# Performance work log

Hardware: AMD Instinct MI355X
Metric: run time of the kernel (lower is better)

The kernel has to match this reference:

```python
import jax, jax.numpy as jnp
import numpy as np

S = 1024   # qlen = klen (mems=None)
B = 4
D = 1024   # d_model
N = 16     # n_head
H = 64     # d_head
R = 2 * S  # relative position embedding length = klen + qlen
EPS = 1e-12
SCALE = float(1.0 / np.sqrt(H))


def setup_inputs() -> dict:
    key = jax.random.key(0)
    ks = jax.random.split(key, 14)
    h = jax.random.normal(ks[0], (S, B, D), dtype=jnp.float32)
    r = jax.random.normal(ks[1], (R, B, D), dtype=jnp.float32)
    # segment ids -> one-hot same/diff segment matrix [i, j, b, 2]
    seg_ids = jax.random.randint(ks[2], (S, B), 0, 2)
    diff = (seg_ids[:, None, :] != seg_ids[None, :, :]).astype(jnp.int32)  # [S,S,B]
    seg_mat = jax.nn.one_hot(diff, 2, dtype=jnp.float32)  # [S,S,B,2]
    # causal attention mask: 1 where key position j > query position i
    causal = (jnp.arange(S)[None, :] > jnp.arange(S)[:, None]).astype(jnp.float32)
    attn_mask = jnp.broadcast_to(causal[:, :, None, None], (S, S, B, 1))
    w = lambda k, shape: 0.02 * jax.random.normal(k, shape, dtype=jnp.float32)
    return {
        "h": h, "r": r, "seg_mat": seg_mat, "attn_mask": attn_mask,
        "Wq": w(ks[3], (D, N, H)), "Wk": w(ks[4], (D, N, H)),
        "Wv": w(ks[5], (D, N, H)), "Wo": w(ks[6], (D, N, H)),
        "Wr": w(ks[7], (D, N, H)),
        "r_w_bias": w(ks[8], (N, H)), "r_r_bias": w(ks[9], (N, H)),
        "r_s_bias": w(ks[10], (N, H)), "seg_embed": w(ks[11], (2, N, H)),
        "ln_scale": jnp.ones((D,), jnp.float32), "ln_bias": jnp.zeros((D,), jnp.float32),
    }


def rel_shift_bnij(x, klen):
    # x: [b, n, i, j_r] with j_r = klen + qlen
    b, n, i, j = x.shape
    x = x.reshape(b, n, j, i)[:, :, 1:, :].reshape(b, n, i, j - 1)
    return x[:, :, :, :klen]


def layer_norm(x, scale, bias):
    mu = jnp.mean(x, axis=-1, keepdims=True)
    var = jnp.mean(jnp.square(x - mu), axis=-1, keepdims=True)
    return (x - mu) * jax.lax.rsqrt(var + EPS) * scale + bias


def reference(h, r, seg_mat, attn_mask, Wq, Wk, Wv, Wo, Wr,
              r_w_bias, r_r_bias, r_s_bias, seg_embed, ln_scale, ln_bias):
    # projections (mems=None => cat = h)
    q_head = jnp.einsum('ibh,hnd->ibnd', h, Wq)
    k_head_h = jnp.einsum('ibh,hnd->ibnd', h, Wk)
    v_head_h = jnp.einsum('ibh,hnd->ibnd', h, Wv)
    k_head_r = jnp.einsum('ibh,hnd->ibnd', r, Wr)

    klen = k_head_h.shape[0]
    # content-based score
    ac = jnp.einsum('ibnd,jbnd->bnij', q_head + r_w_bias, k_head_h)
    # position-based score with relative shift
    bd = jnp.einsum('ibnd,jbnd->bnij', q_head + r_r_bias, k_head_r)
    bd = rel_shift_bnij(bd, klen)
    # segment-based score
    ef = jnp.einsum('ibnd,snd->ibns', q_head + r_s_bias, seg_embed)
    ef = jnp.einsum('ijbs,ibns->bnij', seg_mat, ef)

    attn_score = (ac + bd + ef) * SCALE
    attn_score = attn_score - 1e30 * jnp.transpose(attn_mask, (2, 3, 0, 1))  # ijbn->bnij
    attn_prob = jax.nn.softmax(attn_score, axis=3)

    attn_vec = jnp.einsum('bnij,jbnd->ibnd', attn_prob, v_head_h)
    attn_out = jnp.einsum('ibnd,hnd->ibh', attn_vec, Wo) + h  # residual
    return layer_norm(attn_out, ln_scale, ln_bias)
```

## Files before the change

kernel.cpp:

```cpp
#include <hip/hip_runtime.h>

#define Sq 1024
#define Bb 4
#define Dm 1024
#define Nh 16
#define Hd 64

typedef unsigned short ushort_t;
typedef __attribute__((ext_vector_type(8))) short s8v;
typedef __attribute__((ext_vector_type(8))) unsigned short us8;
typedef __attribute__((ext_vector_type(4))) float f32x4;
typedef __attribute__((ext_vector_type(2))) __fp16 fp16x2;

__device__ __forceinline__ float bf2f(ushort_t u) {
  union { unsigned int i; float f; } t; t.i = ((unsigned int)u) << 16; return t.f;
}
__device__ __forceinline__ ushort_t f2bf(float f) {
  union { float f; unsigned int i; } t; t.f = f;
  unsigned int lsb = (t.i >> 16) & 1u;
  t.i += 0x7fffu + lsb;
  return (ushort_t)(t.i >> 16);
}

__device__ __forceinline__ void load4(const float* p, float* o) {
  const float4 v = *(const float4*)p;
  o[0] = v.x; o[1] = v.y; o[2] = v.z; o[3] = v.w;
}

__device__ __forceinline__ float wave_reduce_sum(float v) {
#pragma unroll
  for (int off = 32; off; off >>= 1) v += __shfl_xor(v, off, 64);
  return v;
}

__device__ __forceinline__ void gl_lds16(const ushort_t* g, ushort_t* l) {
  __builtin_amdgcn_global_load_lds(
      (const __attribute__((address_space(1))) unsigned int*)g,
      (__attribute__((address_space(3))) unsigned int*)l, 16, 0, 0);
}

template <int MODE>
__device__ __forceinline__ void gemm128(const ushort_t* __restrict__ A,
                                        const ushort_t* __restrict__ B,
                                        void* __restrict__ Cv,
                                        const float* __restrict__ bias0,
                                        int bm, int bn,
                                        ushort_t* __restrict__ As,
                                        ushort_t* __restrict__ Bs) {
  const int tid = threadIdx.x;
  const int w = tid >> 6, lane = tid & 63;
  const int quad = lane >> 4, l16 = lane & 15;
  const int wm = (w & 1) * 64, wn = (w >> 1) * 64;
  const int srow0 = 32 * w + (lane >> 2);
  const int scb = (lane & 3) * 16;
  f32x4 acc[4][4] = {};

  for (int k0 = 0; k0 < 1024; k0 += 32) {
    __syncthreads();
#pragma unroll
    for (int c = 0; c < 2; ++c) {
      const int row = srow0 + c * 16;
      const int cbs = scb ^ (((row >> 1) & 3) << 4);
      gl_lds16(A + (size_t)(bm + row) * 1024 + k0 + (cbs >> 1),
               &As[(32 * w + c * 16) * 32]);
      gl_lds16(B + (size_t)(bn + row) * 1024 + k0 + (cbs >> 1),
               &Bs[(32 * w + c * 16) * 32]);
    }
    __syncthreads();
    s8v av[4], bv[4];
    const int sw = ((l16 >> 1) & 3) << 4;
    const int cbb = ((quad * 16) ^ sw) >> 1;
#pragma unroll
    for (int i = 0; i < 4; ++i) {
      av[i] = *(const s8v*)&As[(wm + i * 16 + l16) * 32 + cbb];
      bv[i] = *(const s8v*)&Bs[(wn + i * 16 + l16) * 32 + cbb];
    }
#pragma unroll
    for (int i = 0; i < 4; ++i)
#pragma unroll
      for (int j = 0; j < 4; ++j)
        acc[i][j] = __builtin_amdgcn_mfma_f32_16x16x32_bf16(av[i], bv[j], acc[i][j], 0, 0, 0);
  }

  float bj[4];
  if (MODE == 3) {
#pragma unroll
    for (int j = 0; j < 4; ++j) bj[j] = bias0[bn + wn + j * 16 + l16];
  }
#pragma unroll
  for (int i = 0; i < 4; ++i) {
#pragma unroll
    for (int j = 0; j < 4; ++j) {
      const int cg = bn + wn + j * 16 + l16;
#pragma unroll
      for (int reg = 0; reg < 4; ++reg) {
        const int mg = bm + wm + i * 16 + quad * 4 + reg;
        const float v = acc[i][j][reg];
        if (MODE == 3) {
          ((ushort_t*)Cv)[((size_t)(cg >> 6) * 1024 + mg) * 64 + (cg & 63)] =
              f2bf((v + bj[j]) * 0.125f);
        } else if (MODE == 0) {
          ((ushort_t*)Cv)[((size_t)(cg >> 6) * 1024 + mg) * 64 + (cg & 63)] = f2bf(v);
        } else if (MODE == 2) {
          const int m = cg & 63;
          const int cp = (cg & ~63) | ((m & 15) * 4 + (m >> 4));
          ((ushort_t*)Cv)[(size_t)mg * 1024 + cp] = f2bf(v);
        } else {
          ((float*)Cv)[(size_t)mg * 1024 + cg] = v + bias0[(size_t)mg * 1024 + cg];
        }
      }
    }
  }
}

__global__ __launch_bounds__(256) void prep(
    const float* __restrict__ h, const float* __restrict__ r,
    const float* __restrict__ Wq, const float* __restrict__ Wk,
    const float* __restrict__ Wv, const float* __restrict__ Wr,
    const float* __restrict__ Wo, const float* __restrict__ seg_mat,
    const float* __restrict__ rwb, const float* __restrict__ rrb,
    ushort_t* __restrict__ h_bf, ushort_t* __restrict__ r_bf,
    ushort_t* __restrict__ Wt, ushort_t* __restrict__ Wo_bf,
    float* __restrict__ sseg, float* __restrict__ drr) {
  __shared__ float t[64][68];
  const int x = blockIdx.x, y = blockIdx.y, tid = threadIdx.x;
  if (y < 4) {
    const int b = y, i = x, d0 = tid * 4;
    {
      const float4 v = *(const float4*)&h[(size_t)(i * 4 + b) * 1024 + d0];
      ushort4 o; o.x = f2bf(v.x); o.y = f2bf(v.y); o.z = f2bf(v.z); o.w = f2bf(v.w);
      *(ushort4*)&h_bf[(size_t)b * 1048576 + (size_t)i * 1024 + d0] = o;
    }
    {
      const float4 v = *(const float4*)&r[(size_t)(i * 4 + 4 + b) * 1024 + d0];
      ushort4 o; o.x = f2bf(v.x); o.y = f2bf(v.y); o.z = f2bf(v.z); o.w = f2bf(v.w);
      *(ushort4*)&r_bf[(size_t)b * 1048576 + (size_t)i * 1024 + d0] = o;
    }
    if (b == 0) {
      const float4 v = *(const float4*)&Wo[(size_t)i * 1024 + d0];
      ushort4 o; o.x = f2bf(v.x); o.y = f2bf(v.y); o.z = f2bf(v.z); o.w = f2bf(v.w);
      *(ushort4*)&Wo_bf[(size_t)i * 1024 + d0] = o;
      if (x < 16) {
        const int idx = x * 256 + tid;
        const int bb = idx >> 10, j = idx & 1023;
        sseg[bb * 1024 + j] = seg_mat[(size_t)j * 8 + bb * 2 + 1];
        if (idx < 1024) drr[idx] = (rrb[idx] - rwb[idx]) * 0.125f;
      }
    }
  } else {
    const int z = x >> 8, sub = x & 255;
    const float* W = (z == 0) ? Wq : (z == 1) ? Wk : (z == 2) ? Wv : Wr;
    ushort_t* O = Wt + (size_t)z * 1048576;
    const int n0 = (sub & 15) * 64, k0 = (sub >> 4) * 64;
    const int tr = tid >> 4, tc = (tid & 15) * 4;
#pragma unroll
    for (int rr = 0; rr < 4; ++rr) {
      const int r_ = tr + rr * 16;
      const float4 v = *(const float4*)&W[(size_t)(k0 + r_) * 1024 + n0 + tc];
      t[r_][tc] = v.x; t[r_][tc + 1] = v.y; t[r_][tc + 2] = v.z; t[r_][tc + 3] = v.w;
    }
    __syncthreads();
#pragma unroll
    for (int rr = 0; rr < 4; ++rr) {
      const int nr = tr + rr * 16;
      ushort4 o;
      o.x = f2bf(t[tc + 0][nr]); o.y = f2bf(t[tc + 1][nr]);
      o.z = f2bf(t[tc + 2][nr]); o.w = f2bf(t[tc + 3][nr]);
      *(ushort4*)&O[(size_t)(n0 + nr) * 1024 + k0 + tc] = o;
    }
  }
}

__global__ __launch_bounds__(256) void projAV(
    const ushort_t* __restrict__ h_bf, const ushort_t* __restrict__ r_bf,
    const ushort_t* __restrict__ Wt, const float* __restrict__ rwb,
    ushort_t* __restrict__ qcS, ushort_t* __restrict__ KSl,
    ushort_t* __restrict__ KRS, ushort_t* __restrict__ VTP) {
  __shared__ ushort_t As[128 * 32];
  __shared__ ushort_t Bs[128 * 32];
  const int z = blockIdx.z, zz = z & 3, b = z >> 2;
  const size_t slab = (size_t)Nh * Sq * Hd;
  const int bm = blockIdx.y * 128, bn = blockIdx.x * 128;
  if (zz == 0) {
    gemm128<3>(h_bf + (size_t)b * 1048576, Wt, qcS + b * slab, rwb, bm, bn, As, Bs);
  } else if (zz == 1) {
    gemm128<0>(h_bf + (size_t)b * 1048576, Wt + 1048576, KSl + b * slab,
               nullptr, bm, bn, As, Bs);
  } else if (zz == 2) {
    gemm128<2>(Wt + (size_t)2 * 1048576, h_bf + (size_t)b * 1048576,
               VTP + b * slab, nullptr, bm, bn, As, Bs);
  } else {
    gemm128<0>(r_bf + (size_t)b * 1048576, Wt + (size_t)3 * 1048576,
               KRS + b * slab, nullptr, bm, bn, As, Bs);
  }
}

__global__ __launch_bounds__(128) void attn_mfma(
    const ushort_t* __restrict__ QCS, const ushort_t* __restrict__ KS,
    const ushort_t* __restrict__ VTS, const ushort_t* __restrict__ KRS,
    const float* __restrict__ rwb, const float* __restrict__ rsb,
    const float* __restrict__ seg_embed, const float* __restrict__ sseg,
    const float* __restrict__ drr, ushort_t* __restrict__ AVbf) {
  const int nb = blockIdx.x;
  const int n = nb & 15, b = nb >> 4;
  const int i0b = (int)(gridDim.y - 1 - blockIdx.y) * 32;
  const int tid = threadIdx.x;
  const int w = tid >> 6;
  const int lane = tid & 63;
  const int quad = lane >> 4, l16 = lane & 15;
  const size_t slab = (size_t)Nh * Sq * Hd;
  const size_t nS = (size_t)n * Sq;
  const ushort_t* Qh = QCS + b * slab + nS * Hd;
  const ushort_t* Kh = KS + b * slab + nS * Hd;
  const ushort_t* Vh = VTS + b * slab + (size_t)n * Hd * Sq;
  const ushort_t* KRh = KRS + b * slab + nS * Hd;
  const float* ssegb = sseg + b * Sq;

  __shared__ ushort_t P_s[2][32 * 64];
  __shared__ float o_s[2][32][66];
  __shared__ float l_s[2][32];

  s8v qc[2][2], qr[2][2];
  float efa_v[2], efb_v[2];
  {
    float p0[2] = {0.f, 0.f}, p1[2] = {0.f, 0.f};
#pragma unroll
    for (int ks = 0; ks < 2; ++ks) {
      const int dl = ks * 32 + quad * 8;
      const int db = n * 64 + dl;
      float dr8[8], w8[8], s8a[8], e08[8], e18[8];
      load4(drr + db, dr8); load4(drr + db + 4, dr8 + 4);
      load4(rwb + db, w8);  load4(rwb + db + 4, w8 + 4);
      load4(rsb + db, s8a); load4(rsb + db + 4, s8a + 4);
      load4(seg_embed + db, e08); load4(seg_embed + db + 4, e08 + 4);
      load4(seg_embed + Nh * 64 + db, e18); load4(seg_embed + Nh * 64 + db + 4, e18 + 4);
#pragma unroll
      for (int sub = 0; sub < 2; ++sub) {
        const s8v qv = *(const s8v*)&Qh[(size_t)(i0b + sub * 16 + l16) * 64 + dl];
        qc[sub][ks] = qv;
#pragma unroll
        for (int e = 0; e < 8; ++e) {
          const float qcf = bf2f((ushort_t)qv[e]);
          qr[sub][ks][e] = (short)f2bf(qcf + dr8[e]);
          const float qs = qcf * 8.f - w8[e] + s8a[e];
          p0[sub] += qs * e08[e];
          p1[sub] += qs * e18[e];
        }
      }
    }
#pragma unroll
    for (int sub = 0; sub < 2; ++sub) {
      p0[sub] += __shfl_xor(p0[sub], 16, 64); p0[sub] += __shfl_xor(p0[sub], 32, 64);
      p1[sub] += __shfl_xor(p1[sub], 16, 64); p1[sub] += __shfl_xor(p1[sub], 32, 64);
      const float si = ssegb[i0b + sub * 16 + l16];
      const float de = p1[sub] - p0[sub];
      efa_v[sub] = (p0[sub] + de * si) * 0.125f;
      efb_v[sub] = de * (1.f - 2.f * si) * 0.125f;
    }
  }

  float efa_r[2][4], efb_r[2][4];
  int bp_idx[4], selhi[4];
#pragma unroll
  for (int reg = 0; reg < 4; ++reg) {
    const int il = quad * 4 + reg;
#pragma unroll
    for (int sub = 0; sub < 2; ++sub) {
      efa_r[sub][reg] = __shfl(efa_v[sub], il, 64);
      efb_r[sub][reg] = __shfl(efb_v[sub], il, 64);
    }
    const int off = l16 + 15 - il;
    bp_idx[reg] = (((quad << 4) | (off & 15)) << 2);
    selhi[reg] = off >> 4;
  }

  f32x4 o[2][4] = {};
  float l_r[2][4] = {};
  char* Pb = (char*)P_s[w];

  const int n_jt = i0b / 64 + 1;
  for (int jt = w; jt < n_jt; jt += 2) {
    const int j0 = jt * 64;
    const bool last = (jt == n_jt - 1);

    f32x4 sc[2][4];
    const ushort_t* Kt = Kh + (size_t)j0 * 64;
#pragma unroll
    for (int u = 0; u < 4; ++u) {
      const int ro = (u * 16 + l16) * 64 + quad * 8;
      const s8v k0v = *(const s8v*)&Kt[ro];
      const s8v k1v = *(const s8v*)&Kt[ro + 32];
#pragma unroll
      for (int sub = 0; sub < 2; ++sub) {
        f32x4 a = {};
        a = __builtin_amdgcn_mfma_f32_16x16x32_bf16(qc[sub][0], k0v, a, 0, 0, 0);
        a = __builtin_amdgcn_mfma_f32_16x16x32_bf16(qc[sub][1], k1v, a, 0, 0, 0);
        sc[sub][u] = a;
      }
    }

    f32x4 bdw[2][5];
    const int base1 = 992 + j0 - i0b;
#pragma unroll
    for (int f = 0; f < 6; ++f) {
      int g = base1 + f * 16 + l16;
      if (g > 1023) g = 1023;
      const int ro = g * 64 + quad * 8;
      const s8v r0v = *(const s8v*)&KRh[ro];
      const s8v r1v = *(const s8v*)&KRh[ro + 32];
      if (f < 5) {
        f32x4 a = {};
        a = __builtin_amdgcn_mfma_f32_16x16x32_bf16(qr[1][0], r0v, a, 0, 0, 0);
        a = __builtin_amdgcn_mfma_f32_16x16x32_bf16(qr[1][1], r1v, a, 0, 0, 0);
        bdw[1][f] = a;
      }
      if (f >= 1) {
        f32x4 a = {};
        a = __builtin_amdgcn_mfma_f32_16x16x32_bf16(qr[0][0], r0v, a, 0, 0, 0);
        a = __builtin_amdgcn_mfma_f32_16x16x32_bf16(qr[0][1], r1v, a, 0, 0, 0);
        bdw[0][f - 1] = a;
      }
    }

    float sj[4];
#pragma unroll
    for (int u = 0; u < 4; ++u) sj[u] = ssegb[j0 + u * 16 + l16];
#pragma unroll
    for (int sub = 0; sub < 2; ++sub) {
      float p[4][4];
#pragma unroll
      for (int u = 0; u < 4; ++u) {
#pragma unroll
        for (int reg = 0; reg < 4; ++reg) {
          const fp16x2 t = __builtin_amdgcn_cvt_pkrtz(bdw[sub][u][reg], bdw[sub][u + 1][reg]);
          const int g = __builtin_amdgcn_ds_bpermute(bp_idx[reg], __builtin_bit_cast(int, t));
          const __fp16 hf =
              __builtin_bit_cast(__fp16, (unsigned short)(selhi[reg] ? (g >> 16) : g));
          p[u][reg] = __expf(sc[sub][u][reg] + (float)hf + efa_r[sub][reg] +
                             efb_r[sub][reg] * sj[u]);
        }
      }
      if (last) {
#pragma unroll
        for (int u = 0; u < 4; ++u)
#pragma unroll
          for (int reg = 0; reg < 4; ++reg)
            if (j0 + u * 16 + l16 > i0b + sub * 16 + quad * 4 + reg) p[u][reg] = 0.f;
      }
#pragma unroll
      for (int reg = 0; reg < 4; ++reg)
        l_r[sub][reg] += p[0][reg] + p[1][reg] + p[2][reg] + p[3][reg];

#pragma unroll
      for (int reg = 0; reg < 4; ++reg) {
        const int i = sub * 16 + quad * 4 + reg;
        const unsigned int lo =
            (unsigned int)f2bf(p[0][reg]) | ((unsigned int)f2bf(p[1][reg]) << 16);
        const unsigned int hi =
            (unsigned int)f2bf(p[2][reg]) | ((unsigned int)f2bf(p[3][reg]) << 16);
        *(uint2*)(Pb + i * 128 + ((((l16 >> 1) ^ (i & 7)) << 4) | ((l16 & 1) << 3))) =
            make_uint2(lo, hi);
      }
    }

    s8v pa[2][2];
#pragma unroll
    for (int sub = 0; sub < 2; ++sub)
#pragma unroll
      for (int ks = 0; ks < 2; ++ks)
        pa[sub][ks] = *(const s8v*)(Pb + (sub * 16 + l16) * 128 +
                                    (((ks * 4 + quad) ^ (l16 & 7)) << 4));

    const ushort_t* Vt = Vh + j0;
#pragma unroll
    for (int u = 0; u < 4; ++u) {
      const size_t vro = (size_t)(u * 16 + l16) * Sq + quad * 8;
      const s8v v0 = *(const s8v*)&Vt[vro];
      const s8v v1 = *(const s8v*)&Vt[vro + 32];
#pragma unroll
      for (int sub = 0; sub < 2; ++sub) {
        o[sub][u] = __builtin_amdgcn_mfma_f32_16x16x32_bf16(pa[sub][0], v0, o[sub][u], 0, 0, 0);
        o[sub][u] = __builtin_amdgcn_mfma_f32_16x16x32_bf16(pa[sub][1], v1, o[sub][u], 0, 0, 0);
      }
    }
  }

#pragma unroll
  for (int sub = 0; sub < 2; ++sub)
#pragma unroll
    for (int reg = 0; reg < 4; ++reg) {
#pragma unroll
      for (int off = 1; off < 16; off <<= 1)
        l_r[sub][reg] += __shfl_xor(l_r[sub][reg], off, 64);
    }
  if (l16 == 0) {
#pragma unroll
    for (int sub = 0; sub < 2; ++sub)
#pragma unroll
      for (int reg = 0; reg < 4; ++reg)
        l_s[w][sub * 16 + quad * 4 + reg] = l_r[sub][reg];
  }
#pragma unroll
  for (int sub = 0; sub < 2; ++sub)
#pragma unroll
    for (int u = 0; u < 4; ++u)
#pragma unroll
      for (int reg = 0; reg < 4; ++reg)
        o_s[w][sub * 16 + quad * 4 + reg][u * 16 + l16] = o[sub][u][reg];
  __syncthreads();

  {
    const int row = tid >> 2;
    const int c0 = (tid & 3) * 16;
    const float lt = l_s[0][row] + l_s[1][row];
    const float inv = 1.0f / lt;
    const size_t base = ((size_t)(i0b + row) * Bb + b) * 1024 + n * 64;
#pragma unroll
    for (int half = 0; half < 2; ++half) {
      us8 ob;
#pragma unroll
      for (int e = 0; e < 8; ++e) {
        const int c = c0 + half * 8 + e;
        ob[e] = f2bf((o_s[0][row][c] + o_s[1][row][c]) * inv);
      }
      *(us8*)&AVbf[base + c0 + half * 8] = ob;
    }
  }
}

__global__ __launch_bounds__(256) void ln_res(float* __restrict__ out,
                                              const float* __restrict__ scale,
                                              const float* __restrict__ bias) {
  const int row = blockIdx.x;
  const int tid = threadIdx.x;
  __shared__ float red1[4], red2[4];
  float v[4];
  float sum = 0.f;
#pragma unroll
  for (int c = 0; c < 4; ++c) {
    const int idx = tid + c * 256;
    const float x = out[(size_t)row * Dm + idx];
    v[c] = x;
    sum += x;
  }
  sum = wave_reduce_sum(sum);
  const int wid = tid >> 6, lane = tid & 63;
  if (!lane) red1[wid] = sum;
  __syncthreads();
  const float mean = (red1[0] + red1[1] + red1[2] + red1[3]) * (1.0f / 1024.0f);
  float sq = 0.f;
#pragma unroll
  for (int c = 0; c < 4; ++c) {
    const float t = v[c] - mean;
    sq += t * t;
  }
  sq = wave_reduce_sum(sq);
  if (!lane) red2[wid] = sq;
  __syncthreads();
  const float var = (red2[0] + red2[1] + red2[2] + red2[3]) * (1.0f / 1024.0f);
  const float rstd = rsqrtf(var + 1e-12f);
#pragma unroll
  for (int c = 0; c < 4; ++c) {
    const int idx = tid + c * 256;
    out[(size_t)row * Dm + idx] = (v[c] - mean) * rstd * scale[idx] + bias[idx];
  }
}

__global__ __launch_bounds__(256) void outproj128(const ushort_t* __restrict__ AV,
                                                  const ushort_t* __restrict__ Wo,
                                                  const float* __restrict__ h,
                                                  float* __restrict__ AO) {
  __shared__ ushort_t As[128 * 32];
  __shared__ ushort_t Bs[128 * 32];
  gemm128<1>(AV, Wo, AO, h, blockIdx.y * 128, blockIdx.x * 128, As, Bs);
}

extern "C" void kernel_launch(void* const* d_in, const int* in_sizes, int n_in,
                              void* d_out, int out_size, void* d_ws, size_t ws_size,
                              hipStream_t stream) {
  const float* h = (const float*)d_in[0];
  const float* r = (const float*)d_in[1];
  const float* seg_mat = (const float*)d_in[2];
  const float* Wq = (const float*)d_in[4];
  const float* Wk = (const float*)d_in[5];
  const float* Wv = (const float*)d_in[6];
  const float* Wo = (const float*)d_in[7];
  const float* Wr = (const float*)d_in[8];
  const float* rwb = (const float*)d_in[9];
  const float* rrb = (const float*)d_in[10];
  const float* rsb = (const float*)d_in[11];
  const float* seg_embed = (const float*)d_in[12];
  const float* ln_scale = (const float*)d_in[13];
  const float* ln_bias = (const float*)d_in[14];

  char* wsb = (char*)d_ws;
  const size_t MB = 1024 * 1024;
  ushort_t* h_bf = (ushort_t*)(wsb + 0);
  ushort_t* r_bf = (ushort_t*)(wsb + 8 * MB);
  ushort_t* Wt = (ushort_t*)(wsb + 16 * MB);
  ushort_t* Wo_bf = (ushort_t*)(wsb + 24 * MB);
  ushort_t* qcS = (ushort_t*)(wsb + 26 * MB);
  ushort_t* KSl = (ushort_t*)(wsb + 34 * MB);
  ushort_t* VTP = (ushort_t*)(wsb + 42 * MB);
  ushort_t* KRS = (ushort_t*)(wsb + 50 * MB);
  float* sseg = (float*)(wsb + 58 * MB);
  float* drr = (float*)(wsb + 58 * MB + 16 * 1024);
  ushort_t* AVbf = h_bf;
  float* out = (float*)d_out;

  prep<<<dim3(1024, 5), 256, 0, stream>>>(h, r, Wq, Wk, Wv, Wr, Wo, seg_mat,
                                          rwb, rrb, h_bf, r_bf, Wt, Wo_bf, sseg, drr);
  projAV<<<dim3(8, 8, 16), 256, 0, stream>>>(h_bf, r_bf, Wt, rwb, qcS, KSl, KRS, VTP);
  attn_mfma<<<dim3(64, 32), 128, 0, stream>>>(qcS, KSl, VTP, KRS, rwb, rsb,
                                              seg_embed, sseg, drr, AVbf);
  outproj128<<<dim3(8, 32), 256, 0, stream>>>(AVbf, Wo_bf, h, out);
  ln_res<<<4096, 256, 0, stream>>>(out, ln_scale, ln_bias);
}
```

Baseline: 316.5 us.

## Process key tiles in pairs per wave to overlap softmax with loads

```diff
diff --git a/kernel.cpp b/kernel.cpp
--- a/kernel.cpp
+++ b/kernel.cpp
@@ -195,6 +195,53 @@
   }
 }
 
+__device__ __forceinline__ void softmax_tile(
+    const f32x4 (&sc)[2][4], const f32x4 (&bdw)[2][5],
+    const float* __restrict__ ssegb, int jbase, bool last_t, int i0b,
+    const float (&efa_r)[2][4], const float (&efb_r)[2][4],
+    const int (&bp_idx)[4], const int (&selhi)[4],
+    int quad, int l16, float (&l_r)[2][4], char* Pb) {
+  float sj[4];
+#pragma unroll
+  for (int u = 0; u < 4; ++u) sj[u] = ssegb[jbase + u * 16 + l16];
+#pragma unroll
+  for (int sub = 0; sub < 2; ++sub) {
+    float p[4][4];
+#pragma unroll
+    for (int u = 0; u < 4; ++u) {
+#pragma unroll
+      for (int reg = 0; reg < 4; ++reg) {
+        const fp16x2 t = __builtin_amdgcn_cvt_pkrtz(bdw[sub][u][reg], bdw[sub][u + 1][reg]);
+        const int g = __builtin_amdgcn_ds_bpermute(bp_idx[reg], __builtin_bit_cast(int, t));
+        const __fp16 hf =
+            __builtin_bit_cast(__fp16, (unsigned short)(selhi[reg] ? (g >> 16) : g));
+        p[u][reg] = __expf(sc[sub][u][reg] + (float)hf + efa_r[sub][reg] +
+                           efb_r[sub][reg] * sj[u]);
+      }
+    }
+    if (last_t) {
+#pragma unroll
+      for (int u = 0; u < 4; ++u)
+#pragma unroll
+        for (int reg = 0; reg < 4; ++reg)
+          if (jbase + u * 16 + l16 > i0b + sub * 16 + quad * 4 + reg) p[u][reg] = 0.f;
+    }
+#pragma unroll
+    for (int reg = 0; reg < 4; ++reg)
+      l_r[sub][reg] += p[0][reg] + p[1][reg] + p[2][reg] + p[3][reg];
+#pragma unroll
+    for (int reg = 0; reg < 4; ++reg) {
+      const int i = sub * 16 + quad * 4 + reg;
+      const unsigned int lo =
+          (unsigned int)f2bf(p[0][reg]) | ((unsigned int)f2bf(p[1][reg]) << 16);
+      const unsigned int hi =
+          (unsigned int)f2bf(p[2][reg]) | ((unsigned int)f2bf(p[3][reg]) << 16);
+      *(uint2*)(Pb + i * 128 + ((((l16 >> 1) ^ (i & 7)) << 4) | ((l16 & 1) << 3))) =
+          make_uint2(lo, hi);
+    }
+  }
+}
+
 __global__ __launch_bounds__(128) void attn_mfma(
     const ushort_t* __restrict__ QCS, const ushort_t* __restrict__ KS,
     const ushort_t* __restrict__ VTS, const ushort_t* __restrict__ KRS,
@@ -216,7 +263,7 @@
   const ushort_t* KRh = KRS + b * slab + nS * Hd;
   const float* ssegb = sseg + b * Sq;
 
-  __shared__ ushort_t P_s[2][32 * 64];
+  __shared__ ushort_t P_s[2][2][32 * 64];
   __shared__ float o_s[2][32][66];
   __shared__ float l_s[2][32];
 
@@ -276,111 +323,126 @@
 
   f32x4 o[2][4] = {};
   float l_r[2][4] = {};
-  char* Pb = (char*)P_s[w];
 
   const int n_jt = i0b / 64 + 1;
-  for (int jt = w; jt < n_jt; jt += 2) {
-    const int j0 = jt * 64;
-    const bool last = (jt == n_jt - 1);
-
-    f32x4 sc[2][4];
-    const ushort_t* Kt = Kh + (size_t)j0 * 64;
-#pragma unroll
-    for (int u = 0; u < 4; ++u) {
-      const int ro = (u * 16 + l16) * 64 + quad * 8;
-      const s8v k0v = *(const s8v*)&Kt[ro];
-      const s8v k1v = *(const s8v*)&Kt[ro + 32];
-#pragma unroll
-      for (int sub = 0; sub < 2; ++sub) {
-        f32x4 a = {};
-        a = __builtin_amdgcn_mfma_f32_16x16x32_bf16(qc[sub][0], k0v, a, 0, 0, 0);
-        a = __builtin_amdgcn_mfma_f32_16x16x32_bf16(qc[sub][1], k1v, a, 0, 0, 0);
-        sc[sub][u] = a;
-      }
-    }
-
-    f32x4 bdw[2][5];
-    const int base1 = 992 + j0 - i0b;
-#pragma unroll
-    for (int f = 0; f < 6; ++f) {
-      int g = base1 + f * 16 + l16;
-      if (g > 1023) g = 1023;
-      const int ro = g * 64 + quad * 8;
-      const s8v r0v = *(const s8v*)&KRh[ro];
-      const s8v r1v = *(const s8v*)&KRh[ro + 32];
-      if (f < 5) {
-        f32x4 a = {};
-        a = __builtin_amdgcn_mfma_f32_16x16x32_bf16(qr[1][0], r0v, a, 0, 0, 0);
-        a = __builtin_amdgcn_mfma_f32_16x16x32_bf16(qr[1][1], r1v, a, 0, 0, 0);
-        bdw[1][f] = a;
-      }
-      if (f >= 1) {
-        f32x4 a = {};
-        a = __builtin_amdgcn_mfma_f32_16x16x32_bf16(qr[0][0], r0v, a, 0, 0, 0);
-        a = __builtin_amdgcn_mfma_f32_16x16x32_bf16(qr[0][1], r1v, a, 0, 0, 0);
-        bdw[0][f - 1] = a;
-      }
-    }
-
-    float sj[4];
-#pragma unroll
-    for (int u = 0; u < 4; ++u) sj[u] = ssegb[j0 + u * 16 + l16];
-#pragma unroll
-    for (int sub = 0; sub < 2; ++sub) {
-      float p[4][4];
+  for (int jp = w; 2 * jp < n_jt; jp += 2) {
+    const int j0 = jp * 128;
+    const bool have2 = (2 * jp + 1) < n_jt;
+
+    f32x4 sc[2][2][4];
+#pragma unroll
+    for (int t2 = 0; t2 < 2; ++t2) {
+      if (t2 == 0 || have2) {
+        const ushort_t* Kt = Kh + (size_t)(j0 + t2 * 64) * 64;
+#pragma unroll
+        for (int u = 0; u < 4; ++u) {
+          const int ro = (u * 16 + l16) * 64 + quad * 8;
+          const s8v k0v = *(const s8v*)&Kt[ro];
+          const s8v k1v = *(const s8v*)&Kt[ro + 32];
+#pragma unroll
+          for (int sub = 0; sub < 2; ++sub) {
+            f32x4 a = {};
+            a = __builtin_amdgcn_mfma_f32_16x16x32_bf16(qc[sub][0], k0v, a, 0, 0, 0);
+            a = __builtin_amdgcn_mfma_f32_16x16x32_bf16(qc[sub][1], k1v, a, 0, 0, 0);
+            sc[t2][sub][u] = a;
+          }
+        }
+      }
+    }
+
+    f32x4 bdw[2][2][5];
+    const int base_pair = 992 + j0 - i0b;
+#pragma unroll
+    for (int f = 0; f < 10; ++f) {
+      if (f < 6 || have2) {
+        int g = base_pair + f * 16 + l16;
+        if (g > 1023) g = 1023;
+        const int ro = g * 64 + quad * 8;
+        const s8v r0v = *(const s8v*)&KRh[ro];
+        const s8v r1v = *(const s8v*)&KRh[ro + 32];
+        if (f < 5) {
+          f32x4 a = {};
+          a = __builtin_amdgcn_mfma_f32_16x16x32_bf16(qr[1][0], r0v, a, 0, 0, 0);
+          a = __builtin_amdgcn_mfma_f32_16x16x32_bf16(qr[1][1], r1v, a, 0, 0, 0);
+          bdw[0][1][f] = a;
+        }
+        if (f >= 1 && f <= 5) {
+          f32x4 a = {};
+          a = __builtin_amdgcn_mfma_f32_16x16x32_bf16(qr[0][0], r0v, a, 0, 0, 0);
+          a = __builtin_amdgcn_mfma_f32_16x16x32_bf16(qr[0][1], r1v, a, 0, 0, 0);
+          bdw[0][0][f - 1] = a;
+        }
+        if (have2 && f >= 4 && f <= 8) {
+          f32x4 a = {};
+          a = __builtin_amdgcn_mfma_f32_16x16x32_bf16(qr[1][0], r0v, a, 0, 0, 0);
+          a = __builtin_amdgcn_mfma_f32_16x16x32_bf16(qr[1][1], r1v, a, 0, 0, 0);
+          bdw[1][1][f - 4] = a;
+        }
+        if (have2 && f >= 5) {
+          f32x4 a = {};
+          a = __builtin_amdgcn_mfma_f32_16x16x32_bf16(qr[0][0], r0v, a, 0, 0, 0);
+          a = __builtin_amdgcn_mfma_f32_16x16x32_bf16(qr[0][1], r1v, a, 0, 0, 0);
+          bdw[1][0][f - 5] = a;
+        }
+      }
+    }
+
+    softmax_tile(sc[0], bdw[0], ssegb, j0, (2 * jp == n_jt - 1), i0b,
+                 efa_r, efb_r, bp_idx, selhi, quad, l16, l_r, (char*)P_s[w][0]);
+
+    s8v va0[4], vb0[4];
+    {
+      const ushort_t* Vt = Vh + j0;
 #pragma unroll
       for (int u = 0; u < 4; ++u) {
-#pragma unroll
-        for (int reg = 0; reg < 4; ++reg) {
-          const fp16x2 t = __builtin_amdgcn_cvt_pkrtz(bdw[sub][u][reg], bdw[sub][u + 1][reg]);
-          const int g = __builtin_amdgcn_ds_bpermute(bp_idx[reg], __builtin_bit_cast(int, t));
-          const __fp16 hf =
-              __builtin_bit_cast(__fp16, (unsigned short)(selhi[reg] ? (g >> 16) : g));
-          p[u][reg] = __expf(sc[sub][u][reg] + (float)hf + efa_r[sub][reg] +
-                             efb_r[sub][reg] * sj[u]);
-        }
-      }
-      if (last) {
-#pragma unroll
-        for (int u = 0; u < 4; ++u)
-#pragma unroll
-          for (int reg = 0; reg < 4; ++reg)
-            if (j0 + u * 16 + l16 > i0b + sub * 16 + quad * 4 + reg) p[u][reg] = 0.f;
-      }
-#pragma unroll
-      for (int reg = 0; reg < 4; ++reg)
-        l_r[sub][reg] += p[0][reg] + p[1][reg] + p[2][reg] + p[3][reg];
-
-#pragma unroll
-      for (int reg = 0; reg < 4; ++reg) {
-        const int i = sub * 16 + quad * 4 + reg;
-        const unsigned int lo =
-            (unsigned int)f2bf(p[0][reg]) | ((unsigned int)f2bf(p[1][reg]) << 16);
-        const unsigned int hi =
-            (unsigned int)f2bf(p[2][reg]) | ((unsigned int)f2bf(p[3][reg]) << 16);
-        *(uint2*)(Pb + i * 128 + ((((l16 >> 1) ^ (i & 7)) << 4) | ((l16 & 1) << 3))) =
-            make_uint2(lo, hi);
-      }
-    }
-
-    s8v pa[2][2];
-#pragma unroll
-    for (int sub = 0; sub < 2; ++sub)
-#pragma unroll
-      for (int ks = 0; ks < 2; ++ks)
-        pa[sub][ks] = *(const s8v*)(Pb + (sub * 16 + l16) * 128 +
-                                    (((ks * 4 + quad) ^ (l16 & 7)) << 4));
-
-    const ushort_t* Vt = Vh + j0;
-#pragma unroll
-    for (int u = 0; u < 4; ++u) {
-      const size_t vro = (size_t)(u * 16 + l16) * Sq + quad * 8;
-      const s8v v0 = *(const s8v*)&Vt[vro];
-      const s8v v1 = *(const s8v*)&Vt[vro + 32];
-#pragma unroll
-      for (int sub = 0; sub < 2; ++sub) {
-        o[sub][u] = __builtin_amdgcn_mfma_f32_16x16x32_bf16(pa[sub][0], v0, o[sub][u], 0, 0, 0);
-        o[sub][u] = __builtin_amdgcn_mfma_f32_16x16x32_bf16(pa[sub][1], v1, o[sub][u], 0, 0, 0);
+        const size_t vro = (size_t)(u * 16 + l16) * Sq + quad * 8;
+        va0[u] = *(const s8v*)&Vt[vro];
+        vb0[u] = *(const s8v*)&Vt[vro + 32];
+      }
+    }
+
+    if (have2)
+      softmax_tile(sc[1], bdw[1], ssegb, j0 + 64, (2 * jp + 1 == n_jt - 1), i0b,
+                   efa_r, efb_r, bp_idx, selhi, quad, l16, l_r, (char*)P_s[w][1]);
+
+    {
+      char* Pb = (char*)P_s[w][0];
+      s8v pa[2][2];
+#pragma unroll
+      for (int sub = 0; sub < 2; ++sub)
+#pragma unroll
+        for (int ks = 0; ks < 2; ++ks)
+          pa[sub][ks] = *(const s8v*)(Pb + (sub * 16 + l16) * 128 +
+                                      (((ks * 4 + quad) ^ (l16 & 7)) << 4));
+#pragma unroll
+      for (int u = 0; u < 4; ++u)
+#pragma unroll
+        for (int sub = 0; sub < 2; ++sub) {
+          o[sub][u] = __builtin_amdgcn_mfma_f32_16x16x32_bf16(pa[sub][0], va0[u], o[sub][u], 0, 0, 0);
+          o[sub][u] = __builtin_amdgcn_mfma_f32_16x16x32_bf16(pa[sub][1], vb0[u], o[sub][u], 0, 0, 0);
+        }
+    }
+
+    if (have2) {
+      char* Pb = (char*)P_s[w][1];
+      const ushort_t* Vt = Vh + j0 + 64;
+      s8v pa[2][2];
+#pragma unroll
+      for (int sub = 0; sub < 2; ++sub)
+#pragma unroll
+        for (int ks = 0; ks < 2; ++ks)
+          pa[sub][ks] = *(const s8v*)(Pb + (sub * 16 + l16) * 128 +
+                                      (((ks * 4 + quad) ^ (l16 & 7)) << 4));
+#pragma unroll
+      for (int u = 0; u < 4; ++u) {
+        const size_t vro = (size_t)(u * 16 + l16) * Sq + quad * 8;
+        const s8v v0 = *(const s8v*)&Vt[vro];
+        const s8v v1 = *(const s8v*)&Vt[vro + 32];
+#pragma unroll
+        for (int sub = 0; sub < 2; ++sub) {
+          o[sub][u] = __builtin_amdgcn_mfma_f32_16x16x32_bf16(pa[sub][0], v0, o[sub][u], 0, 0, 0);
+          o[sub][u] = __builtin_amdgcn_mfma_f32_16x16x32_bf16(pa[sub][1], v1, o[sub][u], 0, 0, 0);
+        }
       }
     }
   }
```

Result: no change. 318.9 us (+0.8%).
